# Performance work log

Hardware: AMD Instinct MI355X
Metric: run time of the kernel (lower is better)

The kernel has to match this reference:

```python
import jax, jax.numpy as jnp
import numpy as np

N_NODES = 50000
NEG_SLOPE = 0.2  # DGL GATConv default


def _leaky_relu(x):
    return jnp.where(x >= 0, x, NEG_SLOPE * x)


def gat_conv(h, W, al, ar, src, dst, activate):
    # h: [N, F_in], W: [F_in, H, D], al/ar: [H, D]
    fs = jnp.einsum('nf,fhd->nhd', h, W)          # [N, H, D]
    el = jnp.sum(fs * al, axis=-1)                 # [N, H]
    er = jnp.sum(fs * ar, axis=-1)                 # [N, H]
    e = _leaky_relu(el[src] + er[dst])             # [E, H]
    # numerically stable edge softmax per destination node
    m = jax.ops.segment_max(e, dst, num_segments=N_NODES)   # [N, H]
    ex = jnp.exp(e - m[dst])                                  # [E, H]
    s = jax.ops.segment_sum(ex, dst, num_segments=N_NODES)  # [N, H]
    alpha = ex / s[dst]                                       # [E, H]
    msg = alpha[:, :, None] * fs[src]                          # [E, H, D]
    out = jax.ops.segment_sum(msg, dst, num_segments=N_NODES) # [N, H, D]
    if activate:
        out = jax.nn.relu(out)
    return out


def setup_inputs() -> dict:
    key = jax.random.key(0)
    ks = jax.random.split(key, 12)
    E = 1600000
    H, D, Fin, C = 4, 32, 100, 47
    inp = {
        'x': jax.random.normal(ks[0], (N_NODES, Fin), jnp.float32),
        'W0': jax.random.normal(ks[1], (Fin, H, D), jnp.float32) * 0.1,
        'al0': jax.random.normal(ks[2], (H, D), jnp.float32) * 0.1,
        'ar0': jax.random.normal(ks[3], (H, D), jnp.float32) * 0.1,
        'W1': jax.random.normal(ks[4], (H * D, H, D), jnp.float32) * 0.1,
        'al1': jax.random.normal(ks[5], (H, D), jnp.float32) * 0.1,
        'ar1': jax.random.normal(ks[6], (H, D), jnp.float32) * 0.1,
        'W2': jax.random.normal(ks[7], (H * D, H, C), jnp.float32) * 0.1,
        'al2': jax.random.normal(ks[8], (H, C), jnp.float32) * 0.1,
        'ar2': jax.random.normal(ks[9], (H, C), jnp.float32) * 0.1,
        'src': jax.random.randint(ks[10], (E,), 0, N_NODES, jnp.int32),
        'dst': jax.random.randint(ks[11], (E,), 0, N_NODES, jnp.int32),
    }
    return inp


def reference(x, W0, al0, ar0, W1, al1, ar1, W2, al2, ar2, src, dst):
    h = gat_conv(x, W0, al0, ar0, src, dst, True)            # [N, H, D]
    h = h.reshape(h.shape[0], -1)                             # flatten(1)
    h = gat_conv(h, W1, al1, ar1, src, dst, True)
    h = h.reshape(h.shape[0], -1)
    h = gat_conv(h, W2, al2, ar2, src, dst, False)           # [N, H, C]
    h = h.mean(axis=1)                                        # mean over heads
    return jax.nn.log_softmax(h, axis=-1)                     # [N, C]
```

## Files before the change

kernel.cpp:

```cpp
#include <hip/hip_runtime.h>
#include <hip/hip_bf16.h>


using bf16 = __hip_bfloat16;
typedef __attribute__((ext_vector_type(8))) short short8;
typedef __attribute__((ext_vector_type(4))) float floatx4;

static constexpr int NN = 50000;
static constexpr int H  = 4;

__device__ __forceinline__ float b2f(bf16 x) { return __bfloat162float(x); }
__device__ __forceinline__ float ldx(const void* p, size_t i, bool bf) {
    return bf ? __bfloat162float(((const bf16*)p)[i]) : ((const float*)p)[i];
}
__device__ __forceinline__ unsigned short f2b_bits(float v) {
    bf16 h = __float2bfloat16(v);
    return *reinterpret_cast<unsigned short*>(&h);
}
__device__ __forceinline__ unsigned short w_bits(const void* p, size_t i, bool bf) {
    if (bf) return ((const unsigned short*)p)[i];
    return f2b_bits(((const float*)p)[i]);
}
__device__ __forceinline__ float bl(unsigned u) { return __uint_as_float(u << 16); }
__device__ __forceinline__ float bh(unsigned u) { return __uint_as_float(u & 0xFFFF0000u); }

__global__ void detect_k(const void* __restrict__ x, int* __restrict__ flag) {
    __shared__ int cnt;
    if (threadIdx.x == 0) cnt = 0;
    __syncthreads();
    const unsigned short* u = (const unsigned short*)x;
    unsigned short b = u[threadIdx.x * 2];
    int e = (b >> 7) & 0xFF;
    if (e >= 0x70 && e <= 0x8F) atomicAdd(&cnt, 1);
    __syncthreads();
    if (threadIdx.x == 0) *flag = (cnt > 128) ? 1 : 0;
}

__global__ void xpad_k(const void* __restrict__ x, bf16* __restrict__ xp,
                       const int* __restrict__ flag, int total) {
    int i = blockIdx.x * 256 + threadIdx.x;
    if (i >= total) return;
    const bool bf = (*flag != 0);
    int n = i >> 7, k = i & 127;
    float v = (k < 100) ? ldx(x, (size_t)n * 100 + k, bf) : 0.f;
    xp[i] = __float2bfloat16(v);
}

__global__ void zero_i_k(int* __restrict__ p, int n) {
    int i = blockIdx.x * 256 + threadIdx.x;
    if (i < n) p[i] = 0;
}

__global__ void deg_k(const int* __restrict__ dst, int* __restrict__ deg, int E) {
    int e = blockIdx.x * 256 + threadIdx.x;
    if (e < E) atomicAdd(&deg[dst[e]], 1);
}

__global__ void scan1_k(const int* __restrict__ deg, int* __restrict__ rowptr,
                        int* __restrict__ bsum, int N) {
    __shared__ int buf[256];
    int tid = threadIdx.x, i = blockIdx.x * 256 + tid;
    int v = (i < N) ? deg[i] : 0;
    buf[tid] = v;
    __syncthreads();
    for (int off = 1; off < 256; off <<= 1) {
        int t = (tid >= off) ? buf[tid - off] : 0;
        __syncthreads();
        buf[tid] += t;
        __syncthreads();
    }
    if (i < N) rowptr[i] = buf[tid] - v;
    if (tid == 255) bsum[blockIdx.x] = buf[255];
}

__global__ void scan2_k(const int* __restrict__ bsum, int* __restrict__ boff, int nb) {
    __shared__ int buf[256];
    int tid = threadIdx.x;
    int v = (tid < nb) ? bsum[tid] : 0;
    buf[tid] = v;
    __syncthreads();
    for (int off = 1; off < 256; off <<= 1) {
        int t = (tid >= off) ? buf[tid - off] : 0;
        __syncthreads();
        buf[tid] += t;
        __syncthreads();
    }
    if (tid < nb) boff[tid] = buf[tid] - v;
}

__global__ void scan3_k(int* __restrict__ rowptr, const int* __restrict__ boff,
                        int N, int E) {
    int i = blockIdx.x * 256 + threadIdx.x;
    if (i < N) rowptr[i] += boff[blockIdx.x];
    if (i == 0) rowptr[N] = E;
}

__global__ void fill_k(const int* __restrict__ src, const int* __restrict__ dst,
                       const int* __restrict__ rowptr, int* __restrict__ cur,
                       int* __restrict__ col, int E) {
    int e = blockIdx.x * 256 + threadIdx.x;
    if (e >= E) return;
    int d = dst[e];
    int p = atomicAdd(&cur[d], 1);
    col[rowptr[d] + p] = src[e];
}

template <int KW, int M, int S, int HS, int HW>
__global__ void __launch_bounds__(256) gemm_k(const bf16* __restrict__ in,
                                              const void* __restrict__ W,
                                              const void* __restrict__ al,
                                              const void* __restrict__ ar,
                                              bf16* __restrict__ fs,
                                              float* __restrict__ el,
                                              float* __restrict__ er,
                                              const int* __restrict__ flag, int N) {
    constexpr int CT  = S / 16;
    constexpr int WST = 136;
    __shared__ short wlds[S * WST];
    const bool bf = (*flag != 0);
    const int tid = threadIdx.x;

    for (int idx = tid; idx < 64 * S; idx += 256) {
        int k2 = idx / S, p = idx % S;
        int j = p % HS, h = p / HS;
        int c = h * HW + j;
        bool valid = (j < HW);
        int k0 = 2 * k2;
        unsigned short u0 = (valid && k0 < KW)     ? w_bits(W, (size_t)k0 * M + c, bf)       : 0;
        unsigned short u1 = (valid && k0 + 1 < KW) ? w_bits(W, (size_t)(k0 + 1) * M + c, bf) : 0;
        *(unsigned*)&wlds[p * WST + 2 * k2] = (unsigned)u0 | ((unsigned)u1 << 16);
    }
    __syncthreads();

    const int wave = tid >> 6, lane = tid & 63;
    const int q = lane >> 4, l16 = lane & 15;
    const int tile_base = blockIdx.x * 64 + wave * 16;
    const int node_a = tile_base + l16;

    floatx4 acc[CT] = {};

#pragma unroll
    for (int chunk = 0; chunk < 4; ++chunk) {
        const int kb = chunk * 32 + q * 8;
        short8 a = {};
        if (node_a < N) a = *(const short8*)(in + (size_t)node_a * 128 + kb);
#pragma unroll
        for (int ct = 0; ct < CT; ++ct) {
            const int p = ct * 16 + l16;
            short8 b = *(const short8*)&wlds[p * WST + kb];
            acc[ct] = __builtin_amdgcn_mfma_f32_16x16x32_bf16(a, b, acc[ct], 0, 0, 0);
        }
    }

#pragma unroll
    for (int ct = 0; ct < CT; ++ct) {
        const int p = ct * 16 + l16;
#pragma unroll
        for (int r = 0; r < 4; ++r) {
            int node = tile_base + q * 4 + r;
            if (node < N) fs[(size_t)node * S + p] = __float2bfloat16(acc[ct][r]);
        }
    }

    __syncthreads();
    float* red = (float*)wlds;
    float elp[4][4] = {}, erp[4][4] = {};
#pragma unroll
    for (int ct = 0; ct < CT; ++ct) {
        const int p = ct * 16 + l16;
        const int j = p % HS, h = p / HS;
        const bool valid = (j < HW);
        float alc = valid ? ldx(al, h * HW + j, bf) : 0.f;
        float arc = valid ? ldx(ar, h * HW + j, bf) : 0.f;
#pragma unroll
        for (int r = 0; r < 4; ++r) {
            float v = acc[ct][r];
#pragma unroll
            for (int h2 = 0; h2 < 4; ++h2) {
                elp[r][h2] += (h == h2) ? v * alc : 0.f;
                erp[r][h2] += (h == h2) ? v * arc : 0.f;
            }
        }
    }
#pragma unroll
    for (int r = 0; r < 4; ++r)
#pragma unroll
        for (int h2 = 0; h2 < 4; ++h2) {
            int slot = (wave * 128) + (q * 32) + (r * 8) + (h2 * 2);
            red[slot * 16 + l16] = elp[r][h2];
            red[(slot + 1) * 16 + l16] = erp[r][h2];
        }
    __syncthreads();
#pragma unroll
    for (int pass = 0; pass < 2; ++pass) {
        int slot = tid + pass * 256;
        float sum = 0.f;
#pragma unroll
        for (int j = 0; j < 16; ++j) sum += red[slot * 16 + j];
        int which = slot & 1;
        int h2 = (slot >> 1) & 3;
        int r  = (slot >> 3) & 3;
        int qq = (slot >> 5) & 3;
        int wv = slot >> 7;
        int node = blockIdx.x * 64 + wv * 16 + qq * 4 + r;
        if (node < N) {
            if (which == 0) el[(size_t)node * 4 + h2] = sum;
            else            er[(size_t)node * 4 + h2] = sum;
        }
    }
}

template <int HS, int S, int LPG, int TPB, bool RELU>
__global__ void __launch_bounds__(TPB) agg_k(const float* __restrict__ el,
                                             const float* __restrict__ er,
                                             const bf16* __restrict__ fs,
                                             const int* __restrict__ rowptr,
                                             const int* __restrict__ col,
                                             bf16* __restrict__ out) {
    constexpr int NG = TPB / LPG;
    constexpr int CH = TPB / 4;
    constexpr int NW = TPB / 64;
    const int d = blockIdx.x;
    const int tid = threadIdx.x;
    const int rs = rowptr[d], re = rowptr[d + 1];

    __shared__ float wrow[CH][4];
    __shared__ int scol_s[CH];
    __shared__ float part[NG][S];
    __shared__ float red2[NW][4];
    __shared__ float sh_s[4];

    if (re == rs) {
        if (tid < S / 4) *(uint2*)(out + (size_t)d * S + tid * 4) = make_uint2(0, 0);
        return;
    }

    float4 er4 = *(const float4*)(er + (size_t)d * 4);
    float er_d[4] = {er4.x, er4.y, er4.z, er4.w};

    const int g  = tid / LPG;
    const int lg = tid % LPG;
    const int c0 = lg * 8;
    const int h0 = c0 / HS;

    float acc[8] = {0, 0, 0, 0, 0, 0, 0, 0};
    float swpart = 0.f;

    for (int cs = rs; cs < re; cs += CH) {
        int ne = min(CH, re - cs);
        if (tid < ne * 4) {
            int j = tid >> 2, h = tid & 3;
            int s = col[cs + j];
            if (h == 0) scol_s[j] = s;
            float x = el[(size_t)s * 4 + h] + er_d[h];
            x = x >= 0.f ? x : 0.2f * x;
            float w = __expf(x);
            wrow[j][h] = w;
            swpart += w;
        }
        __syncthreads();
#pragma unroll 4
        for (int e = g; e < ne; e += NG) {
            int s = scol_s[e];
            uint4 u = *(const uint4*)(fs + (size_t)s * S + c0);
            float w = wrow[e][h0];
            acc[0] += w * bl(u.x); acc[1] += w * bh(u.x);
            acc[2] += w * bl(u.y); acc[3] += w * bh(u.y);
            acc[4] += w * bl(u.z); acc[5] += w * bh(u.z);
            acc[6] += w * bl(u.w); acc[7] += w * bh(u.w);
        }
        __syncthreads();
    }

    float sw = swpart;
#pragma unroll
    for (int off = 4; off < 64; off <<= 1) sw += __shfl_xor(sw, off);
    const int wave = tid >> 6, lane = tid & 63;
    if (lane < 4) red2[wave][lane] = sw;
#pragma unroll
    for (int k = 0; k < 8; ++k) part[g][c0 + k] = acc[k];
    __syncthreads();
    if (tid < 4) {
        float s = 0.f;
#pragma unroll
        for (int w = 0; w < NW; ++w) s += red2[w][tid];
        sh_s[tid] = s;
    }
    __syncthreads();

    if (tid < S / 4) {
        int c = tid * 4;
        float4 v = make_float4(0, 0, 0, 0);
#pragma unroll
        for (int gg = 0; gg < NG; ++gg) {
            v.x += part[gg][c + 0]; v.y += part[gg][c + 1];
            v.z += part[gg][c + 2]; v.w += part[gg][c + 3];
        }
        float is = 1.0f / sh_s[c / HS];
        v.x *= is; v.y *= is; v.z *= is; v.w *= is;
        if (RELU) {
            v.x = fmaxf(v.x, 0.f); v.y = fmaxf(v.y, 0.f);
            v.z = fmaxf(v.z, 0.f); v.w = fmaxf(v.w, 0.f);
        }
        unsigned p0 = (unsigned)f2b_bits(v.x) | ((unsigned)f2b_bits(v.y) << 16);
        unsigned p1 = (unsigned)f2b_bits(v.z) | ((unsigned)f2b_bits(v.w) << 16);
        *(uint2*)(out + (size_t)d * S + c) = make_uint2(p0, p1);
    }
}

__global__ void __launch_bounds__(192) agg2_k(const float* __restrict__ el,
                                              const float* __restrict__ er,
                                              const bf16* __restrict__ fs,
                                              const int* __restrict__ rowptr,
                                              const int* __restrict__ col,
                                              void* __restrict__ out,
                                              const int* __restrict__ flag) {
    constexpr int HS = 48, S = 192, LPG = 24, TPB = 192;
    constexpr int NG = TPB / LPG;
    constexpr int CH = TPB / 4;
    constexpr int NW = TPB / 64;
    const int d = blockIdx.x;
    const int tid = threadIdx.x;
    const bool bf = (*flag != 0);
    const int rs = rowptr[d], re = rowptr[d + 1];

    __shared__ float wrow[CH][4];
    __shared__ int scol_s[CH];
    __shared__ float part[NG][S];
    __shared__ float red2[NW][4];
    __shared__ float sh_s[4];
    __shared__ float vout[S];

    if (re == rs) {
        if (tid < 47) {
            float r = -logf(47.f);
            if (bf) ((bf16*)out)[(size_t)d * 47 + tid] = __float2bfloat16(r);
            else    ((float*)out)[(size_t)d * 47 + tid] = r;
        }
        return;
    }

    float4 er4 = *(const float4*)(er + (size_t)d * 4);
    float er_d[4] = {er4.x, er4.y, er4.z, er4.w};

    const int g  = tid / LPG;
    const int lg = tid % LPG;
    const int c0 = lg * 8;
    const int h0 = c0 / HS;

    float acc[8] = {0, 0, 0, 0, 0, 0, 0, 0};
    float swpart = 0.f;

    for (int cs = rs; cs < re; cs += CH) {
        int ne = min(CH, re - cs);
        if (tid < ne * 4) {
            int j = tid >> 2, h = tid & 3;
            int s = col[cs + j];
            if (h == 0) scol_s[j] = s;
            float x = el[(size_t)s * 4 + h] + er_d[h];
            x = x >= 0.f ? x : 0.2f * x;
            float w = __expf(x);
            wrow[j][h] = w;
            swpart += w;
        }
        __syncthreads();
#pragma unroll 4
        for (int e = g; e < ne; e += NG) {
            int s = scol_s[e];
            uint4 u = *(const uint4*)(fs + (size_t)s * S + c0);
            float w = wrow[e][h0];
            acc[0] += w * bl(u.x); acc[1] += w * bh(u.x);
            acc[2] += w * bl(u.y); acc[3] += w * bh(u.y);
            acc[4] += w * bl(u.z); acc[5] += w * bh(u.z);
            acc[6] += w * bl(u.w); acc[7] += w * bh(u.w);
        }
        __syncthreads();
    }

    float sw = swpart;
#pragma unroll
    for (int off = 4; off < 64; off <<= 1) sw += __shfl_xor(sw, off);
    const int wave = tid >> 6, lane = tid & 63;
    if (lane < 4) red2[wave][lane] = sw;
#pragma unroll
    for (int k = 0; k < 8; ++k) part[g][c0 + k] = acc[k];
    __syncthreads();
    if (tid < 4) {
        float s = 0.f;
#pragma unroll
        for (int w = 0; w < NW; ++w) s += red2[w][tid];
        sh_s[tid] = s;
    }
    __syncthreads();

    if (tid < S / 4) {
        int c = tid * 4;
        float4 v = make_float4(0, 0, 0, 0);
#pragma unroll
        for (int gg = 0; gg < NG; ++gg) {
            v.x += part[gg][c + 0]; v.y += part[gg][c + 1];
            v.z += part[gg][c + 2]; v.w += part[gg][c + 3];
        }
        float is = 1.0f / sh_s[c / HS];
        vout[c + 0] = v.x * is; vout[c + 1] = v.y * is;
        vout[c + 2] = v.z * is; vout[c + 3] = v.w * is;
    }
    __syncthreads();

    if (tid < 64) {
        int c = tid;
        float val = 0.f, vm = -INFINITY;
        if (c < 47) {
            val = 0.25f * (vout[c] + vout[48 + c] + vout[96 + c] + vout[144 + c]);
            vm = val;
        }
        float m = vm;
#pragma unroll
        for (int off = 32; off >= 1; off >>= 1) m = fmaxf(m, __shfl_xor(m, off));
        float ex = (c < 47) ? __expf(val - m) : 0.f;
        float s = ex;
#pragma unroll
        for (int off = 32; off >= 1; off >>= 1) s += __shfl_xor(s, off);
        if (c < 47) {
            float r = val - m - logf(s);
            if (bf) ((bf16*)out)[(size_t)d * 47 + c] = __float2bfloat16(r);
            else    ((float*)out)[(size_t)d * 47 + c] = r;
        }
    }
}

extern "C" void kernel_launch(void* const* d_in, const int* in_sizes, int n_in,
                              void* d_out, int out_size, void* d_ws, size_t ws_size,
                              hipStream_t stream) {
    const void* x   = d_in[0];
    const void* W0  = d_in[1];
    const void* al0 = d_in[2];
    const void* ar0 = d_in[3];
    const void* W1  = d_in[4];
    const void* al1 = d_in[5];
    const void* ar1 = d_in[6];
    const void* W2  = d_in[7];
    const void* al2 = d_in[8];
    const void* ar2 = d_in[9];
    const int* src  = (const int*)d_in[10];
    const int* dst  = (const int*)d_in[11];
    const int E = in_sizes[10];
    const int N = NN;

    bf16* fs    = (bf16*)d_ws;
    bf16* hb16  = fs + (size_t)N * 192;
    bf16* xpad  = hb16 + (size_t)N * 128;
    float* el   = (float*)(xpad + (size_t)N * 128);
    float* er   = el + (size_t)N * H;
    int* rowptr = (int*)(er + (size_t)N * H);
    int* cur    = rowptr + (N + 1);
    int* col    = cur + N;
    int* bsum   = col + E;
    int* boff   = bsum + 256;
    int* flag   = boff + 256;

    const int gN = (N + 255) / 256;
    const int gE = (E + 255) / 256;
    const int gG = (N + 63) / 64;

    detect_k<<<1, 256, 0, stream>>>(x, flag);
    xpad_k<<<(N * 128 + 255) / 256, 256, 0, stream>>>(x, xpad, flag, N * 128);

    zero_i_k<<<gN, 256, 0, stream>>>(cur, N);
    deg_k<<<gE, 256, 0, stream>>>(dst, cur, E);
    scan1_k<<<gN, 256, 0, stream>>>(cur, rowptr, bsum, N);
    scan2_k<<<1, 256, 0, stream>>>(bsum, boff, gN);
    scan3_k<<<gN, 256, 0, stream>>>(rowptr, boff, N, E);
    zero_i_k<<<gN, 256, 0, stream>>>(cur, N);
    fill_k<<<gE, 256, 0, stream>>>(src, dst, rowptr, cur, col, E);

    gemm_k<100, 128, 128, 32, 32><<<gG, 256, 0, stream>>>(
        xpad, W0, al0, ar0, fs, el, er, flag, N);
    agg_k<32, 128, 16, 256, true><<<N, 256, 0, stream>>>(el, er, fs, rowptr, col, hb16);

    gemm_k<128, 128, 128, 32, 32><<<gG, 256, 0, stream>>>(
        hb16, W1, al1, ar1, fs, el, er, flag, N);
    agg_k<32, 128, 16, 256, true><<<N, 256, 0, stream>>>(el, er, fs, rowptr, col, hb16);

    gemm_k<128, 188, 192, 48, 47><<<gG, 256, 0, stream>>>(
        hb16, W2, al2, ar2, fs, el, er, flag, N);
    agg2_k<<<N, 192, 0, stream>>>(el, er, fs, rowptr, col, d_out, flag);
}
```

Baseline: 644.6 us.

## Aggregate one destination node per wavefront and double GEMM rows per block

The layer-0/1 aggregation kernel now maps each destination node to a single 64-lane wavefront, four nodes per block. Partial sums are reduced with cross-lane shuffles instead of shared memory and block-wide barriers. This removes per-node block launch overhead and the __syncthreads cost on nodes with about 32 edges. The GEMM kernel now computes 128 nodes per block so each LDS weight load is reused across two row tiles, and zero-init kernels are replaced by hipMemsetAsync. The trade-off is more accumulator registers in the GEMM and serial edge chunks of 16 per wave.

```diff
diff --git a/kernel.cpp b/kernel.cpp
--- a/kernel.cpp
+++ b/kernel.cpp
@@ -44,11 +44,6 @@
     int n = i >> 7, k = i & 127;
     float v = (k < 100) ? ldx(x, (size_t)n * 100 + k, bf) : 0.f;
     xp[i] = __float2bfloat16(v);
-}
-
-__global__ void zero_i_k(int* __restrict__ p, int n) {
-    int i = blockIdx.x * 256 + threadIdx.x;
-    if (i < n) p[i] = 0;
 }
 
 __global__ void deg_k(const int* __restrict__ dst, int* __restrict__ deg, int E) {
@@ -134,177 +129,169 @@
 
     const int wave = tid >> 6, lane = tid & 63;
     const int q = lane >> 4, l16 = lane & 15;
-    const int tile_base = blockIdx.x * 64 + wave * 16;
-    const int node_a = tile_base + l16;
-
-    floatx4 acc[CT] = {};
+    const int base = blockIdx.x * 128;
+
+    floatx4 acc[2][CT] = {};
 
 #pragma unroll
     for (int chunk = 0; chunk < 4; ++chunk) {
         const int kb = chunk * 32 + q * 8;
-        short8 a = {};
-        if (node_a < N) a = *(const short8*)(in + (size_t)node_a * 128 + kb);
+        short8 a0 = {}, a1 = {};
+        const int n0 = base + wave * 16 + l16;
+        const int n1 = n0 + 64;
+        if (n0 < N) a0 = *(const short8*)(in + (size_t)n0 * 128 + kb);
+        if (n1 < N) a1 = *(const short8*)(in + (size_t)n1 * 128 + kb);
 #pragma unroll
         for (int ct = 0; ct < CT; ++ct) {
             const int p = ct * 16 + l16;
             short8 b = *(const short8*)&wlds[p * WST + kb];
-            acc[ct] = __builtin_amdgcn_mfma_f32_16x16x32_bf16(a, b, acc[ct], 0, 0, 0);
-        }
-    }
-
-#pragma unroll
-    for (int ct = 0; ct < CT; ++ct) {
-        const int p = ct * 16 + l16;
-#pragma unroll
-        for (int r = 0; r < 4; ++r) {
-            int node = tile_base + q * 4 + r;
-            if (node < N) fs[(size_t)node * S + p] = __float2bfloat16(acc[ct][r]);
-        }
-    }
-
-    __syncthreads();
+            acc[0][ct] = __builtin_amdgcn_mfma_f32_16x16x32_bf16(a0, b, acc[0][ct], 0, 0, 0);
+            acc[1][ct] = __builtin_amdgcn_mfma_f32_16x16x32_bf16(a1, b, acc[1][ct], 0, 0, 0);
+        }
+    }
+
+#pragma unroll
+    for (int rt = 0; rt < 2; ++rt) {
+        const int tb = base + rt * 64 + wave * 16;
+#pragma unroll
+        for (int ct = 0; ct < CT; ++ct) {
+            const int p = ct * 16 + l16;
+#pragma unroll
+            for (int r = 0; r < 4; ++r) {
+                int node = tb + q * 4 + r;
+                if (node < N) fs[(size_t)node * S + p] = __float2bfloat16(acc[rt][ct][r]);
+            }
+        }
+    }
+
     float* red = (float*)wlds;
-    float elp[4][4] = {}, erp[4][4] = {};
-#pragma unroll
-    for (int ct = 0; ct < CT; ++ct) {
-        const int p = ct * 16 + l16;
-        const int j = p % HS, h = p / HS;
-        const bool valid = (j < HW);
-        float alc = valid ? ldx(al, h * HW + j, bf) : 0.f;
-        float arc = valid ? ldx(ar, h * HW + j, bf) : 0.f;
-#pragma unroll
-        for (int r = 0; r < 4; ++r) {
-            float v = acc[ct][r];
+#pragma unroll
+    for (int rt = 0; rt < 2; ++rt) {
+        __syncthreads();
+        float elp[4][4] = {}, erp[4][4] = {};
+#pragma unroll
+        for (int ct = 0; ct < CT; ++ct) {
+            const int p = ct * 16 + l16;
+            const int j = p % HS, h = p / HS;
+            const bool valid = (j < HW);
+            float alc = valid ? ldx(al, h * HW + j, bf) : 0.f;
+            float arc = valid ? ldx(ar, h * HW + j, bf) : 0.f;
+#pragma unroll
+            for (int r = 0; r < 4; ++r) {
+                float v = acc[rt][ct][r];
+#pragma unroll
+                for (int h2 = 0; h2 < 4; ++h2) {
+                    elp[r][h2] += (h == h2) ? v * alc : 0.f;
+                    erp[r][h2] += (h == h2) ? v * arc : 0.f;
+                }
+            }
+        }
+#pragma unroll
+        for (int r = 0; r < 4; ++r)
 #pragma unroll
             for (int h2 = 0; h2 < 4; ++h2) {
-                elp[r][h2] += (h == h2) ? v * alc : 0.f;
-                erp[r][h2] += (h == h2) ? v * arc : 0.f;
+                int slot = (wave * 128) + (q * 32) + (r * 8) + (h2 * 2);
+                red[slot * 16 + l16] = elp[r][h2];
+                red[(slot + 1) * 16 + l16] = erp[r][h2];
             }
-        }
-    }
-#pragma unroll
-    for (int r = 0; r < 4; ++r)
-#pragma unroll
-        for (int h2 = 0; h2 < 4; ++h2) {
-            int slot = (wave * 128) + (q * 32) + (r * 8) + (h2 * 2);
-            red[slot * 16 + l16] = elp[r][h2];
-            red[(slot + 1) * 16 + l16] = erp[r][h2];
-        }
-    __syncthreads();
-#pragma unroll
-    for (int pass = 0; pass < 2; ++pass) {
-        int slot = tid + pass * 256;
-        float sum = 0.f;
-#pragma unroll
-        for (int j = 0; j < 16; ++j) sum += red[slot * 16 + j];
-        int which = slot & 1;
-        int h2 = (slot >> 1) & 3;
-        int r  = (slot >> 3) & 3;
-        int qq = (slot >> 5) & 3;
-        int wv = slot >> 7;
-        int node = blockIdx.x * 64 + wv * 16 + qq * 4 + r;
-        if (node < N) {
-            if (which == 0) el[(size_t)node * 4 + h2] = sum;
-            else            er[(size_t)node * 4 + h2] = sum;
-        }
-    }
-}
-
-template <int HS, int S, int LPG, int TPB, bool RELU>
-__global__ void __launch_bounds__(TPB) agg_k(const float* __restrict__ el,
-                                             const float* __restrict__ er,
-                                             const bf16* __restrict__ fs,
-                                             const int* __restrict__ rowptr,
-                                             const int* __restrict__ col,
-                                             bf16* __restrict__ out) {
-    constexpr int NG = TPB / LPG;
-    constexpr int CH = TPB / 4;
-    constexpr int NW = TPB / 64;
-    const int d = blockIdx.x;
-    const int tid = threadIdx.x;
+        __syncthreads();
+#pragma unroll
+        for (int pass = 0; pass < 2; ++pass) {
+            int slot = tid + pass * 256;
+            float sum = 0.f;
+#pragma unroll
+            for (int j = 0; j < 16; ++j) sum += red[slot * 16 + j];
+            int which = slot & 1;
+            int h2 = (slot >> 1) & 3;
+            int r  = (slot >> 3) & 3;
+            int qq = (slot >> 5) & 3;
+            int wv = slot >> 7;
+            int node = base + rt * 64 + wv * 16 + qq * 4 + r;
+            if (node < N) {
+                if (which == 0) el[(size_t)node * 4 + h2] = sum;
+                else            er[(size_t)node * 4 + h2] = sum;
+            }
+        }
+    }
+}
+
+template <bool RELU>
+__global__ void __launch_bounds__(256) agg01_k(const float* __restrict__ el,
+                                               const float* __restrict__ er,
+                                               const bf16* __restrict__ fs,
+                                               const int* __restrict__ rowptr,
+                                               const int* __restrict__ col,
+                                               bf16* __restrict__ out, int N) {
+    const int wave = threadIdx.x >> 6, lane = threadIdx.x & 63;
+    const int d = blockIdx.x * 4 + wave;
+    __shared__ float wrow[4][16][4];
+    __shared__ int   scol[4][16];
+    if (d >= N) return;
     const int rs = rowptr[d], re = rowptr[d + 1];
-
-    __shared__ float wrow[CH][4];
-    __shared__ int scol_s[CH];
-    __shared__ float part[NG][S];
-    __shared__ float red2[NW][4];
-    __shared__ float sh_s[4];
+    const int g = lane >> 4, lg = lane & 15;
+    const int c0 = lg * 8;
 
     if (re == rs) {
-        if (tid < S / 4) *(uint2*)(out + (size_t)d * S + tid * 4) = make_uint2(0, 0);
+        if (g == 0) *(uint4*)(out + (size_t)d * 128 + c0) = make_uint4(0, 0, 0, 0);
         return;
     }
 
     float4 er4 = *(const float4*)(er + (size_t)d * 4);
     float er_d[4] = {er4.x, er4.y, er4.z, er4.w};
 
-    const int g  = tid / LPG;
-    const int lg = tid % LPG;
-    const int c0 = lg * 8;
-    const int h0 = c0 / HS;
+    const int eh = lane >> 2;
+    const int hh = lane & 3;
+    const int h0 = lg >> 2;
 
     float acc[8] = {0, 0, 0, 0, 0, 0, 0, 0};
-    float swpart = 0.f;
-
-    for (int cs = rs; cs < re; cs += CH) {
-        int ne = min(CH, re - cs);
-        if (tid < ne * 4) {
-            int j = tid >> 2, h = tid & 3;
-            int s = col[cs + j];
-            if (h == 0) scol_s[j] = s;
-            float x = el[(size_t)s * 4 + h] + er_d[h];
+    float swp = 0.f;
+
+    for (int cs = rs; cs < re; cs += 16) {
+        int ne = min(16, re - cs);
+        if (eh < ne) {
+            int s = col[cs + eh];
+            if (hh == 0) scol[wave][eh] = s;
+            float x = el[(size_t)s * 4 + hh] + er_d[hh];
             x = x >= 0.f ? x : 0.2f * x;
             float w = __expf(x);
-            wrow[j][h] = w;
-            swpart += w;
-        }
-        __syncthreads();
+            wrow[wave][eh][hh] = w;
+            swp += w;
+        }
 #pragma unroll 4
-        for (int e = g; e < ne; e += NG) {
-            int s = scol_s[e];
-            uint4 u = *(const uint4*)(fs + (size_t)s * S + c0);
-            float w = wrow[e][h0];
+        for (int e = g; e < ne; e += 4) {
+            int s = scol[wave][e];
+            float w = wrow[wave][e][h0];
+            uint4 u = *(const uint4*)(fs + (size_t)s * 128 + c0);
             acc[0] += w * bl(u.x); acc[1] += w * bh(u.x);
             acc[2] += w * bl(u.y); acc[3] += w * bh(u.y);
             acc[4] += w * bl(u.z); acc[5] += w * bh(u.z);
             acc[6] += w * bl(u.w); acc[7] += w * bh(u.w);
         }
-        __syncthreads();
-    }
-
-    float sw = swpart;
-#pragma unroll
-    for (int off = 4; off < 64; off <<= 1) sw += __shfl_xor(sw, off);
-    const int wave = tid >> 6, lane = tid & 63;
-    if (lane < 4) red2[wave][lane] = sw;
-#pragma unroll
-    for (int k = 0; k < 8; ++k) part[g][c0 + k] = acc[k];
-    __syncthreads();
-    if (tid < 4) {
-        float s = 0.f;
-#pragma unroll
-        for (int w = 0; w < NW; ++w) s += red2[w][tid];
-        sh_s[tid] = s;
-    }
-    __syncthreads();
-
-    if (tid < S / 4) {
-        int c = tid * 4;
-        float4 v = make_float4(0, 0, 0, 0);
-#pragma unroll
-        for (int gg = 0; gg < NG; ++gg) {
-            v.x += part[gg][c + 0]; v.y += part[gg][c + 1];
-            v.z += part[gg][c + 2]; v.w += part[gg][c + 3];
-        }
-        float is = 1.0f / sh_s[c / HS];
-        v.x *= is; v.y *= is; v.z *= is; v.w *= is;
-        if (RELU) {
-            v.x = fmaxf(v.x, 0.f); v.y = fmaxf(v.y, 0.f);
-            v.z = fmaxf(v.z, 0.f); v.w = fmaxf(v.w, 0.f);
-        }
-        unsigned p0 = (unsigned)f2b_bits(v.x) | ((unsigned)f2b_bits(v.y) << 16);
-        unsigned p1 = (unsigned)f2b_bits(v.z) | ((unsigned)f2b_bits(v.w) << 16);
-        *(uint2*)(out + (size_t)d * S + c) = make_uint2(p0, p1);
+    }
+
+#pragma unroll
+    for (int k = 0; k < 8; ++k) {
+        acc[k] += __shfl_xor(acc[k], 16);
+        acc[k] += __shfl_xor(acc[k], 32);
+    }
+#pragma unroll
+    for (int off = 4; off < 64; off <<= 1) swp += __shfl_xor(swp, off);
+    float sh = __shfl(swp, h0);
+
+    if (g == 0) {
+        float inv = 1.0f / sh;
+        float v[8];
+#pragma unroll
+        for (int k = 0; k < 8; ++k) {
+            v[k] = acc[k] * inv;
+            if (RELU) v[k] = fmaxf(v[k], 0.f);
+        }
+        uint4 o;
+        o.x = (unsigned)f2b_bits(v[0]) | ((unsigned)f2b_bits(v[1]) << 16);
+        o.y = (unsigned)f2b_bits(v[2]) | ((unsigned)f2b_bits(v[3]) << 16);
+        o.z = (unsigned)f2b_bits(v[4]) | ((unsigned)f2b_bits(v[5]) << 16);
+        o.w = (unsigned)f2b_bits(v[6]) | ((unsigned)f2b_bits(v[7]) << 16);
+        *(uint4*)(out + (size_t)d * 128 + c0) = o;
     }
 }
 
@@ -459,28 +446,29 @@
     int* boff   = bsum + 256;
     int* flag   = boff + 256;
 
-    const int gN = (N + 255) / 256;
-    const int gE = (E + 255) / 256;
-    const int gG = (N + 63) / 64;
+    const int gN  = (N + 255) / 256;
+    const int gE  = (E + 255) / 256;
+    const int gG  = (N + 127) / 128;
+    const int gA  = (N + 3) / 4;
 
     detect_k<<<1, 256, 0, stream>>>(x, flag);
     xpad_k<<<(N * 128 + 255) / 256, 256, 0, stream>>>(x, xpad, flag, N * 128);
 
-    zero_i_k<<<gN, 256, 0, stream>>>(cur, N);
+    hipMemsetAsync(cur, 0, (size_t)N * 4, stream);
     deg_k<<<gE, 256, 0, stream>>>(dst, cur, E);
     scan1_k<<<gN, 256, 0, stream>>>(cur, rowptr, bsum, N);
     scan2_k<<<1, 256, 0, stream>>>(bsum, boff, gN);
     scan3_k<<<gN, 256, 0, stream>>>(rowptr, boff, N, E);
-    zero_i_k<<<gN, 256, 0, stream>>>(cur, N);
+    hipMemsetAsync(cur, 0, (size_t)N * 4, stream);
     fill_k<<<gE, 256, 0, stream>>>(src, dst, rowptr, cur, col, E);
 
     gemm_k<100, 128, 128, 32, 32><<<gG, 256, 0, stream>>>(
         xpad, W0, al0, ar0, fs, el, er, flag, N);
-    agg_k<32, 128, 16, 256, true><<<N, 256, 0, stream>>>(el, er, fs, rowptr, col, hb16);
+    agg01_k<true><<<gA, 256, 0, stream>>>(el, er, fs, rowptr, col, hb16, N);
 
     gemm_k<128, 128, 128, 32, 32><<<gG, 256, 0, stream>>>(
         hb16, W1, al1, ar1, fs, el, er, flag, N);
-    agg_k<32, 128, 16, 256, true><<<N, 256, 0, stream>>>(el, er, fs, rowptr, col, hb16);
+    agg01_k<true><<<gA, 256, 0, stream>>>(el, er, fs, rowptr, col, hb16, N);
 
     gemm_k<128, 188, 192, 48, 47><<<gG, 256, 0, stream>>>(
         hb16, W2, al2, ar2, fs, el, er, flag, N);
```

Result: faster. 598.3 us (-7.2%).
